# Kernel optimization log

Hardware: AMD Instinct MI355X
Metric: run time of the kernel (lower is better)

Reference implementation:

```python
import jax, jax.numpy as jnp
import numpy as np

N = 50000
E = 800000
IN_C = 128
HID = 32
OUT_C = 16
NEG_SLOPE = 0.2


def setup_inputs() -> dict:
    key = jax.random.key(0)
    ks = jax.random.split(key, 16)
    x = jax.random.normal(ks[0], (N, IN_C), dtype=jnp.float32)
    edge_index = jax.random.randint(ks[1], (2, E), 0, N, dtype=jnp.int64)

    def glorot(k, shape):
        fan = shape[0] + shape[-1]
        return jax.random.uniform(k, shape, jnp.float32, -1.0, 1.0) * jnp.sqrt(6.0 / fan)

    # layer1: in=128 -> heads=4, ch=32, concat -> out 128
    W1 = glorot(ks[2], (IN_C, 4 * HID))
    a_src1 = glorot(ks[3], (4, HID))
    a_dst1 = glorot(ks[4], (4, HID))
    b1 = jnp.zeros((4 * HID,), jnp.float32)
    # layer2: in=128 -> heads=2, ch=32, concat -> out 64
    W2 = glorot(ks[5], (4 * HID, 2 * HID))
    a_src2 = glorot(ks[6], (2, HID))
    a_dst2 = glorot(ks[7], (2, HID))
    b2 = jnp.zeros((2 * HID,), jnp.float32)
    # layer3: in=64 -> heads=1, ch=16, mean -> out 16
    W3 = glorot(ks[8], (2 * HID, OUT_C))
    a_src3 = glorot(ks[9], (1, OUT_C))
    a_dst3 = glorot(ks[10], (1, OUT_C))
    b3 = jnp.zeros((OUT_C,), jnp.float32)
    return {"x": x, "edge_index": edge_index,
            "W1": W1, "a_src1": a_src1, "a_dst1": a_dst1, "b1": b1,
            "W2": W2, "a_src2": a_src2, "a_dst2": a_dst2, "b2": b2,
            "W3": W3, "a_src3": a_src3, "a_dst3": a_dst3, "b3": b3}


def gat_conv(x, src, dst, W, a_src, a_dst, bias, heads, ch, concat):
    n = x.shape[0]
    h = (x @ W).reshape(n, heads, ch)                      # [N,H,C]
    alpha_s = jnp.einsum('nhc,hc->nh', h, a_src)           # [N,H]
    alpha_d = jnp.einsum('nhc,hc->nh', h, a_dst)           # [N,H]
    logits = jax.nn.leaky_relu(alpha_s[src] + alpha_d[dst], NEG_SLOPE)  # [E,H]
    # segment softmax over edges sharing the same destination node
    m = jax.ops.segment_max(logits, dst, num_segments=n)
    m = jnp.where(jnp.isfinite(m), m, 0.0)
    e = jnp.exp(logits - m[dst])
    denom = jax.ops.segment_sum(e, dst, num_segments=n)
    alpha = e / (denom[dst] + 1e-16)                       # [E,H]
    msg = h[src] * alpha[:, :, None]                       # [E,H,C]
    out = jax.ops.segment_sum(msg, dst, num_segments=n)    # [N,H,C]
    out = out.reshape(n, heads * ch) if concat else out.mean(axis=1)
    return out + bias


def reference(x, edge_index, W1, a_src1, a_dst1, b1, W2, a_src2, a_dst2, b2, W3, a_src3, a_dst3, b3):
    n = x.shape[0]
    loops = jnp.arange(n, dtype=edge_index.dtype)
    src = jnp.concatenate([edge_index[0], loops])  # add self loops (PyG default)
    dst = jnp.concatenate([edge_index[1], loops])
    h = jax.nn.relu(gat_conv(x, src, dst, W1, a_src1, a_dst1, b1, 4, HID, True))
    h = jax.nn.relu(gat_conv(h, src, dst, W2, a_src2, a_dst2, b2, 2, HID, True))
    out = gat_conv(h, src, dst, W3, a_src3, a_dst3, b3, 1, OUT_C, False)
    return out
```

## Files before the change

kernel.cpp:

```cpp
#include <hip/hip_runtime.h>
#include <hip/hip_bf16.h>
#include <stdint.h>

#define NODES 50000
#define NEDGE 800000
#define TEDGE (NEDGE + NODES)

typedef unsigned short u16;
typedef unsigned int u32;
typedef unsigned long long u64;
typedef short s16x8 __attribute__((ext_vector_type(8)));
typedef float f32x4 __attribute__((ext_vector_type(4)));

__device__ __forceinline__ float bf2f(u16 v) {
  return __uint_as_float(((u32)v) << 16);
}
__device__ __forceinline__ u16 f2bf(float f) {
  u32 u = __float_as_uint(f);
  u32 r = (u + 0x7FFFu + ((u >> 16) & 1u)) >> 16;
  return (u16)r;
}
__device__ __forceinline__ float lo16f(u32 w) { return __uint_as_float(w << 16); }
__device__ __forceinline__ float hi16f(u32 w) { return __uint_as_float(w & 0xFFFF0000u); }
__device__ __forceinline__ float lrelu(float x) {
  return (x > 0.f) ? x : 0.2f * x;
}
__device__ __forceinline__ int clampn(int v) {
  return ((u32)v < NODES) ? v : 0;
}
__device__ __forceinline__ float load1(const void* p, size_t i, bool fb) {
  return fb ? bf2f(((const u16*)p)[i]) : ((const float*)p)[i];
}
__device__ __forceinline__ u32 encf(float f) {
  u32 u = __float_as_uint(f);
  return (u & 0x80000000u) ? ~u : (u | 0x80000000u);
}
__device__ __forceinline__ float decf(u32 k) {
  u32 u = (k & 0x80000000u) ? (k & 0x7FFFFFFFu) : ~k;
  return __uint_as_float(u);
}

__global__ __launch_bounds__(256) void k_probe(const int* __restrict__ ei,
                                               const u16* __restrict__ xs16,
                                               int* __restrict__ flags,
                                               int* __restrict__ deg) {
  int t = threadIdx.x;
  int g = blockIdx.x * 256 + t;
  if (g < NODES) deg[g] = 0;
  if (blockIdx.x == 0 && t >= 2 && t < 32) flags[t] = 0;
  if (blockIdx.x == 0 && t < 64) {
    int odd = 0, even = 0, big = 0;
#pragma unroll
    for (int k = 0; k < 4; ++k) {
      int idx = t + 64 * k;
      odd |= (ei[2 * idx + 1] != 0);
      even |= (ei[2 * idx] != 0);
      u32 ex = (xs16[2 * (t * 4 + k)] >> 7) & 0xFF;
      big += (ex >= 0x90);
    }
    u64 bo = __ballot(odd);
    u64 be = __ballot(even);
#pragma unroll
    for (int off = 32; off >= 1; off >>= 1) big += __shfl_xor(big, off);
    if (t == 0) {
      flags[0] = (bo == 0ull && be != 0ull) ? 1 : 0;
      flags[1] = (big >= 8) ? 0 : 1;
    }
  }
}


__global__ __launch_bounds__(256) void k_hist(const int* __restrict__ ei,
                                              const int* __restrict__ flags,
                                              int* deg, u16* __restrict__ rankarr,
                                              u16* __restrict__ src16,
                                              u16* __restrict__ dst16,
                                              const void* __restrict__ W1,
                                              const void* __restrict__ W2,
                                              const void* __restrict__ W3,
                                              u16* __restrict__ wt1,
                                              u16* __restrict__ wt2,
                                              u16* __restrict__ wt3) {
  int e = blockIdx.x * 256 + threadIdx.x;
  if (e >= TEDGE) return;
  bool fb = flags[1] != 0;
  if (e < 25600) {
    if (e < 16384) {
      int n = e >> 7, k = e & 127;
      wt1[n * 128 + k] = f2bf(load1(W1, (size_t)k * 128 + n, fb));
    } else if (e < 24576) {
      int r = e - 16384;
      int n = r >> 7, k = r & 127;
      wt2[n * 128 + k] = f2bf(load1(W2, (size_t)k * 64 + n, fb));
    } else {
      int r = e - 24576;
      int n = r >> 6, k = r & 63;
      wt3[n * 64 + k] = f2bf(load1(W3, (size_t)k * 16 + n, fb));
    }
  }
  int d, s;
  if (e < NEDGE) {
    if (flags[0]) { s = ei[2 * e]; d = ei[2 * (NEDGE + e)]; }
    else { s = ei[e]; d = ei[NEDGE + e]; }
  } else {
    s = e - NEDGE; d = s;
  }
  s = clampn(s); d = clampn(d);
  src16[e] = (u16)s;
  dst16[e] = (u16)d;
  int r = atomicAdd(&deg[d], 1);
  rankarr[e] = (u16)min(r, 65535);
}

__global__ __launch_bounds__(1024) void k_scan(const int* __restrict__ deg,
                                               int* __restrict__ rowptr, int n) {
  int t = threadIdx.x, lane = t & 63, w = t >> 6;
  __shared__ int swave[16], soff[17];
  int carry = 0;
  for (int base = 0; base < n; base += 4096) {
    int i0 = base + t * 4;
    int v[4];
#pragma unroll
    for (int j = 0; j < 4; j++) { int i = i0 + j; v[j] = (i < n) ? deg[i] : 0; }
    int local = v[0] + v[1] + v[2] + v[3];
    int x = local;
#pragma unroll
    for (int off = 1; off < 64; off <<= 1) {
      int y = __shfl_up(x, off);
      if (lane >= off) x += y;
    }
    if (lane == 63) swave[w] = x;
    __syncthreads();
    if (w == 0) {
      int wv = (lane < 16) ? swave[lane] : 0;
#pragma unroll
      for (int off = 1; off < 16; off <<= 1) {
        int y = __shfl_up(wv, off);
        if (lane >= off) wv += y;
      }
      if (lane < 16) soff[lane + 1] = wv;
      if (lane == 0) soff[0] = 0;
    }
    __syncthreads();
    int run = carry + soff[w] + (x - local);
#pragma unroll
    for (int j = 0; j < 4; j++) {
      int i = i0 + j;
      if (i < n) rowptr[i] = run;
      run += v[j];
    }
    carry += soff[16];
    __syncthreads();
  }
  if (t == 0) rowptr[n] = carry;
}

__global__ __launch_bounds__(256) void k_scatter(const u16* __restrict__ src16,
                                                 const u16* __restrict__ dst16,
                                                 const int* __restrict__ rowptr,
                                                 const u16* __restrict__ rankarr,
                                                 u16* __restrict__ srcs) {
  int e = blockIdx.x * 256 + threadIdx.x;
  if (e >= TEDGE) return;
  int d = dst16[e];
  int pos = rowptr[d] + (int)rankarr[e];
  srcs[pos] = src16[e];
}


template <int K, int N, int H, bool XEXT>
__global__ __launch_bounds__(256) void k_gmfma(const void* __restrict__ xin,
                                               const u16* __restrict__ wtg,
                                               const void* __restrict__ a_src,
                                               const void* __restrict__ a_dst,
                                               u16* __restrict__ hout,
                                               float* __restrict__ asg,
                                               float* __restrict__ adg,
                                               u32* __restrict__ gm,
                                               const int* __restrict__ flags,
                                               int M) {
  constexpr int KP = K + 8;
  constexpr int NT = N / 16;
  constexpr int NTH = NT / H;
  constexpr int KG = K / 8;
  __shared__ u16 wlds[N * KP];
  __shared__ u16 xlds[64 * KP];
  __shared__ u32 lmax[2 * H];
  int t = threadIdx.x;
  int row0 = blockIdx.x * 64;
  bool fb = flags[1] != 0;
  if (t < 2 * H) lmax[t] = 0;

  for (int i = t; i < N * KG; i += 256) {
    int n = i / KG, kg = i % KG;
    *(uint4*)&wlds[n * KP + kg * 8] = *(const uint4*)(wtg + (size_t)n * K + kg * 8);
  }
  bool xbf = XEXT ? fb : true;
  for (int i = t; i < 64 * KG; i += 256) {
    int r = i / KG, kg = i % KG;
    int grow = row0 + r;
    if (grow >= M) grow = M - 1;
    if (xbf) {
      *(uint4*)&xlds[r * KP + kg * 8] =
          *(const uint4*)((const u16*)xin + (size_t)grow * K + kg * 8);
    } else {
      const float* gp = (const float*)xin + (size_t)grow * K + kg * 8;
      float4 f0 = *(const float4*)gp, f1 = *(const float4*)(gp + 4);
      *(ushort4*)&xlds[r * KP + kg * 8] =
          make_ushort4(f2bf(f0.x), f2bf(f0.y), f2bf(f0.z), f2bf(f0.w));
      *(ushort4*)&xlds[r * KP + kg * 8 + 4] =
          make_ushort4(f2bf(f1.x), f2bf(f1.y), f2bf(f1.z), f2bf(f1.w));
    }
  }
  __syncthreads();

  int lane = t & 63, w = t >> 6;
  int lrow = lane & 15, quad = lane >> 4;
  f32x4 acc[NT];
#pragma unroll
  for (int nt = 0; nt < NT; ++nt) acc[nt] = (f32x4){0.f, 0.f, 0.f, 0.f};

  const u16* xbase = xlds + (w * 16 + lrow) * KP + quad * 8;
  const u16* wbase = wlds + lrow * KP + quad * 8;
#pragma unroll
  for (int ks = 0; ks < K / 32; ++ks) {
    s16x8 a = *(const s16x8*)(xbase + ks * 32);
#pragma unroll
    for (int nt = 0; nt < NT; ++nt) {
      s16x8 b = *(const s16x8*)(wbase + (size_t)nt * 16 * KP + ks * 32);
      acc[nt] = __builtin_amdgcn_mfma_f32_16x16x32_bf16(a, b, acc[nt], 0, 0, 0);
    }
  }

  float avs[NT], avd[NT];
#pragma unroll
  for (int nt = 0; nt < NT; ++nt) {
    avs[nt] = load1(a_src, nt * 16 + lrow, fb);
    avd[nt] = load1(a_dst, nt * 16 + lrow, fb);
  }
  int baserow = row0 + w * 16 + quad * 4;
#pragma unroll
  for (int r = 0; r < 4; ++r) {
    int grow = baserow + r;
    float ps[H], pd[H];
#pragma unroll
    for (int h = 0; h < H; ++h) {
      ps[h] = 0.f; pd[h] = 0.f;
#pragma unroll
      for (int i = 0; i < NTH; ++i) {
        int nt = h * NTH + i;
        ps[h] += acc[nt][r] * avs[nt];
        pd[h] += acc[nt][r] * avd[nt];
      }
    }
#pragma unroll
    for (int m = 1; m < 16; m <<= 1) {
#pragma unroll
      for (int h = 0; h < H; ++h) {
        ps[h] += __shfl_xor(ps[h], m);
        pd[h] += __shfl_xor(pd[h], m);
      }
    }
    if (grow < M) {
#pragma unroll
      for (int nt = 0; nt < NT; ++nt)
        hout[(size_t)grow * N + nt * 16 + lrow] = f2bf(acc[nt][r]);
#pragma unroll
      for (int h = 0; h < H; ++h) {
        if (lrow == h) {
          asg[grow * H + h] = ps[h];
          adg[grow * H + h] = pd[h];
          atomicMax(&lmax[h], encf(ps[h]));
          atomicMax(&lmax[H + h], encf(pd[h]));
        }
      }
    }
  }
  __syncthreads();
  if (t < 2 * H) atomicMax(&gm[t], lmax[t]);
}


template <int H, int C, bool RELU, bool FINAL>
__global__ __launch_bounds__(256) void k_agg(const u16* __restrict__ hbuf,
                                             const float* __restrict__ asg,
                                             const float* __restrict__ adg,
                                             const int* __restrict__ rowptr,
                                             const u16* __restrict__ srcs,
                                             const void* __restrict__ bias,
                                             const int* __restrict__ flags,
                                             const u32* __restrict__ gm,
                                             void* __restrict__ outp, int n) {
  constexpr int HC = H * C;
  constexpr int L = HC / 8;
  constexpr int EPN = 32 / L;
  constexpr int UN = (4 * EPN <= 32) ? 4 : 2;
  __shared__ u16 lds_s[4][64];
  __shared__ float lds_e[4][64][H];
  int lane = threadIdx.x & 63;
  int w = threadIdx.x >> 6;
  int nh = lane >> 5;
  int hl = lane & 31;
  int node = blockIdx.x * 8 + w * 2 + nh;
  if (node >= n) node = n - 1;
  bool fb = flags[1] != 0;
  int start = rowptr[node], end = rowptr[node + 1];
  if (end < start || end - start > TEDGE) { start = 0; end = 0; }

  float adh[H], M[H];
#pragma unroll
  for (int h = 0; h < H; ++h) adh[h] = adg[node * H + h];
#pragma unroll
  for (int h = 0; h < H; ++h) M[h] = lrelu(decf(gm[h]) + decf(gm[H + h]));

  int sub = hl / L;
  int cl = hl & (L - 1);
  int ch0 = cl * 8;
  int myhead = ch0 / C;
  int base = nh * 32;

  float den[H];
#pragma unroll
  for (int h = 0; h < H; ++h) den[h] = 0.f;
  float acc[UN][8];
#pragma unroll
  for (int u = 0; u < UN; ++u)
#pragma unroll
    for (int i = 0; i < 8; ++i) acc[u][i] = 0.f;

  for (int chunk = start; chunk < end; chunk += 32) {
    int e = chunk + hl;
    int s = 0;
    float ee[H];
#pragma unroll
    for (int h = 0; h < H; ++h) ee[h] = 0.f;
    if (e < end) {
      s = srcs[e];
      float av[H];
      if (H == 4) { float4 t4 = *(const float4*)(asg + s * 4);
        av[0] = t4.x; av[1] = t4.y; av[H > 2 ? 2 : 0] = t4.z; av[H > 3 ? 3 : 0] = t4.w; }
      else if (H == 2) { float2 t2 = *(const float2*)(asg + s * 2); av[0] = t2.x; av[1] = t2.y; }
      else av[0] = asg[s];
#pragma unroll
      for (int h = 0; h < H; ++h) {
        float x = __expf(lrelu(av[h] + adh[h]) - M[h]);
        ee[h] = x;
        den[h] += x;
      }
    }
    __builtin_amdgcn_wave_barrier();
    lds_s[w][lane] = (u16)s;
#pragma unroll
    for (int h = 0; h < H; ++h) lds_e[w][lane][h] = ee[h];
    __builtin_amdgcn_wave_barrier();

    int cn = min(32, end - chunk);
    for (int j = 0; j < cn; j += UN * EPN) {
      int sx[UN];
      float ax[UN];
#pragma unroll
      for (int u = 0; u < UN; ++u) {
        int ei_ = base + j + u * EPN + sub;
        sx[u] = lds_s[w][ei_];
        ax[u] = lds_e[w][ei_][myhead];
      }
#pragma unroll
      for (int u = 0; u < UN; ++u) {
        uint4 v = *(const uint4*)(hbuf + (size_t)sx[u] * HC + ch0);
        acc[u][0] += ax[u] * lo16f(v.x); acc[u][1] += ax[u] * hi16f(v.x);
        acc[u][2] += ax[u] * lo16f(v.y); acc[u][3] += ax[u] * hi16f(v.y);
        acc[u][4] += ax[u] * lo16f(v.z); acc[u][5] += ax[u] * hi16f(v.z);
        acc[u][6] += ax[u] * lo16f(v.w); acc[u][7] += ax[u] * hi16f(v.w);
      }
    }
  }

#pragma unroll
  for (int m = 16; m >= 1; m >>= 1) {
#pragma unroll
    for (int h = 0; h < H; ++h) den[h] += __shfl_xor(den[h], m);
  }
  float tt[8];
#pragma unroll
  for (int i = 0; i < 8; ++i) {
    tt[i] = acc[0][i];
#pragma unroll
    for (int u = 1; u < UN; ++u) tt[i] += acc[u][i];
  }
#pragma unroll
  for (int m = L; m < 32; m <<= 1) {
#pragma unroll
    for (int i = 0; i < 8; ++i) tt[i] += __shfl_xor(tt[i], m);
  }

  if (sub == 0) {
    float inv = 1.f / (den[myhead] + 1e-16f);
    float o[8];
#pragma unroll
    for (int i = 0; i < 8; ++i) {
      o[i] = tt[i] * inv + load1(bias, ch0 + i, fb);
      if (RELU) o[i] = fmaxf(o[i], 0.f);
    }
    bool obf = FINAL ? fb : true;
    if (obf) {
      uint4 pk;
      pk.x = (u32)f2bf(o[0]) | ((u32)f2bf(o[1]) << 16);
      pk.y = (u32)f2bf(o[2]) | ((u32)f2bf(o[3]) << 16);
      pk.z = (u32)f2bf(o[4]) | ((u32)f2bf(o[5]) << 16);
      pk.w = (u32)f2bf(o[6]) | ((u32)f2bf(o[7]) << 16);
      *(uint4*)((u16*)outp + (size_t)node * HC + ch0) = pk;
    } else {
      float* op = (float*)outp + (size_t)node * HC + ch0;
      *(float4*)op = make_float4(o[0], o[1], o[2], o[3]);
      *(float4*)(op + 4) = make_float4(o[4], o[5], o[6], o[7]);
    }
  }
}


extern "C" void kernel_launch(void* const* d_in, const int* in_sizes, int n_in,
                              void* d_out, int out_size, void* d_ws, size_t ws_size,
                              hipStream_t stream) {
  const void* x   = d_in[0];
  const int* ei   = (const int*)d_in[1];
  const void* W1  = d_in[2];
  const void* as1 = d_in[3];
  const void* ad1 = d_in[4];
  const void* b1  = d_in[5];
  const void* W2  = d_in[6];
  const void* as2 = d_in[7];
  const void* ad2 = d_in[8];
  const void* b2  = d_in[9];
  const void* W3  = d_in[10];
  const void* as3 = d_in[11];
  const void* ad3 = d_in[12];
  const void* b3  = d_in[13];

  char* w = (char*)d_ws;
  auto alloc = [&](size_t bytes) {
    char* p = w;
    w += (bytes + 255) & ~(size_t)255;
    return p;
  };
  int* flags    = (int*)alloc(256);
  int* deg      = (int*)alloc((size_t)NODES * 4);
  int* rowptr   = (int*)alloc((size_t)(NODES + 1) * 4);
  u16* rankarr  = (u16*)alloc((size_t)TEDGE * 2);
  u16* src16    = (u16*)alloc((size_t)TEDGE * 2);
  u16* dst16    = (u16*)alloc((size_t)TEDGE * 2);
  u16* srcs     = (u16*)alloc((size_t)TEDGE * 2);
  float* asg    = (float*)alloc((size_t)NODES * 4 * 4);
  float* adg    = (float*)alloc((size_t)NODES * 4 * 4);
  u16* wt1      = (u16*)alloc((size_t)128 * 128 * 2);
  u16* wt2      = (u16*)alloc((size_t)64 * 128 * 2);
  u16* wt3      = (u16*)alloc((size_t)16 * 64 * 2);
  u16* hbuf     = (u16*)alloc((size_t)NODES * 128 * 2);
  u16* obuf     = (u16*)alloc((size_t)NODES * 128 * 2);

  u32* gm1 = (u32*)(flags + 8);
  u32* gm2 = (u32*)(flags + 16);
  u32* gm3 = (u32*)(flags + 24);

  k_probe<<<(NODES + 255) / 256, 256, 0, stream>>>(ei, (const u16*)x, flags, deg);
  k_hist<<<(TEDGE + 255) / 256, 256, 0, stream>>>(ei, flags, deg, rankarr, src16, dst16,
                                                  W1, W2, W3, wt1, wt2, wt3);
  k_scan<<<1, 1024, 0, stream>>>(deg, rowptr, NODES);
  k_scatter<<<(TEDGE + 255) / 256, 256, 0, stream>>>(src16, dst16, rowptr, rankarr, srcs);

  int gblocks = (NODES + 63) / 64;
  int ablocks = (NODES + 7) / 8;
  k_gmfma<128, 128, 4, true><<<gblocks, 256, 0, stream>>>(x, wt1, as1, ad1, hbuf, asg, adg, gm1, flags, NODES);
  k_agg<4, 32, true, false><<<ablocks, 256, 0, stream>>>(hbuf, asg, adg, rowptr, srcs, b1, flags, gm1, obuf, NODES);
  k_gmfma<128, 64, 2, false><<<gblocks, 256, 0, stream>>>(obuf, wt2, as2, ad2, hbuf, asg, adg, gm2, flags, NODES);
  k_agg<2, 32, true, false><<<ablocks, 256, 0, stream>>>(hbuf, asg, adg, rowptr, srcs, b2, flags, gm2, obuf, NODES);
  k_gmfma<64, 16, 1, false><<<gblocks, 256, 0, stream>>>(obuf, wt3, as3, ad3, hbuf, asg, adg, gm3, flags, NODES);
  k_agg<1, 16, false, true><<<ablocks, 256, 0, stream>>>(hbuf, asg, adg, rowptr, srcs, b3, flags, gm3, d_out, NODES);
}
```

Before: 307.6 us.

## Fuse histogram, scan and layer-1 GEMM into one kernel with spin-wait

Moves the weight transposition into the probe kernel, with each block recomputing the precision flag locally. The edge histogram, the single-block prefix scan and the layer-1 MFMA GEMM now run as one launch. Block 0 spins on an atomic counter until all histogram blocks finish and then scans, so the GEMM tiles run concurrently with the graph build. This removes two launches and the serialized single-block scan from the critical path. It relies on block 0 not starving the histogram blocks while it spins, and uses a 256-thread scan in place of the 1024-thread one.

```diff
diff --git a/kernel.cpp b/kernel.cpp
--- a/kernel.cpp
+++ b/kernel.cpp
@@ -5,6 +5,8 @@
 #define NODES 50000
 #define NEDGE 800000
 #define TEDGE (NEDGE + NODES)
+#define HBLK ((TEDGE + 255) / 256)
+#define GBLK ((NODES + 63) / 64)
 
 typedef unsigned short u16;
 typedef unsigned int u32;
@@ -43,151 +45,80 @@
 __global__ __launch_bounds__(256) void k_probe(const int* __restrict__ ei,
                                                const u16* __restrict__ xs16,
                                                int* __restrict__ flags,
-                                               int* __restrict__ deg) {
+                                               int* __restrict__ deg,
+                                               const void* __restrict__ W1,
+                                               const void* __restrict__ W2,
+                                               const void* __restrict__ W3,
+                                               u16* __restrict__ wt1,
+                                               u16* __restrict__ wt2,
+                                               u16* __restrict__ wt3) {
+  __shared__ int sfb;
   int t = threadIdx.x;
   int g = blockIdx.x * 256 + t;
   if (g < NODES) deg[g] = 0;
   if (blockIdx.x == 0 && t >= 2 && t < 32) flags[t] = 0;
-  if (blockIdx.x == 0 && t < 64) {
-    int odd = 0, even = 0, big = 0;
+  if (t < 64) {
+    int big = 0;
 #pragma unroll
     for (int k = 0; k < 4; ++k) {
-      int idx = t + 64 * k;
-      odd |= (ei[2 * idx + 1] != 0);
-      even |= (ei[2 * idx] != 0);
       u32 ex = (xs16[2 * (t * 4 + k)] >> 7) & 0xFF;
       big += (ex >= 0x90);
     }
-    u64 bo = __ballot(odd);
-    u64 be = __ballot(even);
 #pragma unroll
     for (int off = 32; off >= 1; off >>= 1) big += __shfl_xor(big, off);
-    if (t == 0) {
-      flags[0] = (bo == 0ull && be != 0ull) ? 1 : 0;
-      flags[1] = (big >= 8) ? 0 : 1;
-    }
-  }
-}
-
-
-__global__ __launch_bounds__(256) void k_hist(const int* __restrict__ ei,
-                                              const int* __restrict__ flags,
-                                              int* deg, u16* __restrict__ rankarr,
-                                              u16* __restrict__ src16,
-                                              u16* __restrict__ dst16,
-                                              const void* __restrict__ W1,
-                                              const void* __restrict__ W2,
-                                              const void* __restrict__ W3,
-                                              u16* __restrict__ wt1,
-                                              u16* __restrict__ wt2,
-                                              u16* __restrict__ wt3) {
-  int e = blockIdx.x * 256 + threadIdx.x;
-  if (e >= TEDGE) return;
-  bool fb = flags[1] != 0;
-  if (e < 25600) {
-    if (e < 16384) {
-      int n = e >> 7, k = e & 127;
+    if (t == 0) sfb = (big >= 8) ? 0 : 1;
+    if (blockIdx.x == 0) {
+      int odd = 0, even = 0;
+#pragma unroll
+      for (int k = 0; k < 4; ++k) {
+        int idx = t + 64 * k;
+        odd |= (ei[2 * idx + 1] != 0);
+        even |= (ei[2 * idx] != 0);
+      }
+      u64 bo = __ballot(odd);
+      u64 be = __ballot(even);
+      if (t == 0) flags[0] = (bo == 0ull && be != 0ull) ? 1 : 0;
+    }
+  }
+  __syncthreads();
+  bool fb = sfb != 0;
+  if (blockIdx.x == 0 && t == 0) flags[1] = fb ? 1 : 0;
+  if (g < 25600) {
+    if (g < 16384) {
+      int n = g >> 7, k = g & 127;
       wt1[n * 128 + k] = f2bf(load1(W1, (size_t)k * 128 + n, fb));
-    } else if (e < 24576) {
-      int r = e - 16384;
+    } else if (g < 24576) {
+      int r = g - 16384;
       int n = r >> 7, k = r & 127;
       wt2[n * 128 + k] = f2bf(load1(W2, (size_t)k * 64 + n, fb));
     } else {
-      int r = e - 24576;
+      int r = g - 24576;
       int n = r >> 6, k = r & 63;
       wt3[n * 64 + k] = f2bf(load1(W3, (size_t)k * 16 + n, fb));
     }
   }
-  int d, s;
-  if (e < NEDGE) {
-    if (flags[0]) { s = ei[2 * e]; d = ei[2 * (NEDGE + e)]; }
-    else { s = ei[e]; d = ei[NEDGE + e]; }
-  } else {
-    s = e - NEDGE; d = s;
-  }
-  s = clampn(s); d = clampn(d);
-  src16[e] = (u16)s;
-  dst16[e] = (u16)d;
-  int r = atomicAdd(&deg[d], 1);
-  rankarr[e] = (u16)min(r, 65535);
-}
-
-__global__ __launch_bounds__(1024) void k_scan(const int* __restrict__ deg,
-                                               int* __restrict__ rowptr, int n) {
-  int t = threadIdx.x, lane = t & 63, w = t >> 6;
-  __shared__ int swave[16], soff[17];
-  int carry = 0;
-  for (int base = 0; base < n; base += 4096) {
-    int i0 = base + t * 4;
-    int v[4];
-#pragma unroll
-    for (int j = 0; j < 4; j++) { int i = i0 + j; v[j] = (i < n) ? deg[i] : 0; }
-    int local = v[0] + v[1] + v[2] + v[3];
-    int x = local;
-#pragma unroll
-    for (int off = 1; off < 64; off <<= 1) {
-      int y = __shfl_up(x, off);
-      if (lane >= off) x += y;
-    }
-    if (lane == 63) swave[w] = x;
-    __syncthreads();
-    if (w == 0) {
-      int wv = (lane < 16) ? swave[lane] : 0;
-#pragma unroll
-      for (int off = 1; off < 16; off <<= 1) {
-        int y = __shfl_up(wv, off);
-        if (lane >= off) wv += y;
-      }
-      if (lane < 16) soff[lane + 1] = wv;
-      if (lane == 0) soff[0] = 0;
-    }
-    __syncthreads();
-    int run = carry + soff[w] + (x - local);
-#pragma unroll
-    for (int j = 0; j < 4; j++) {
-      int i = i0 + j;
-      if (i < n) rowptr[i] = run;
-      run += v[j];
-    }
-    carry += soff[16];
-    __syncthreads();
-  }
-  if (t == 0) rowptr[n] = carry;
-}
-
-__global__ __launch_bounds__(256) void k_scatter(const u16* __restrict__ src16,
-                                                 const u16* __restrict__ dst16,
-                                                 const int* __restrict__ rowptr,
-                                                 const u16* __restrict__ rankarr,
-                                                 u16* __restrict__ srcs) {
-  int e = blockIdx.x * 256 + threadIdx.x;
-  if (e >= TEDGE) return;
-  int d = dst16[e];
-  int pos = rowptr[d] + (int)rankarr[e];
-  srcs[pos] = src16[e];
 }
 
 
 template <int K, int N, int H, bool XEXT>
-__global__ __launch_bounds__(256) void k_gmfma(const void* __restrict__ xin,
-                                               const u16* __restrict__ wtg,
-                                               const void* __restrict__ a_src,
-                                               const void* __restrict__ a_dst,
-                                               u16* __restrict__ hout,
-                                               float* __restrict__ asg,
-                                               float* __restrict__ adg,
-                                               u32* __restrict__ gm,
-                                               const int* __restrict__ flags,
-                                               int M) {
+__device__ __forceinline__ void gmfma_tile(const void* __restrict__ xin,
+                                           const u16* __restrict__ wtg,
+                                           const void* __restrict__ a_src,
+                                           const void* __restrict__ a_dst,
+                                           u16* __restrict__ hout,
+                                           float* __restrict__ asg,
+                                           float* __restrict__ adg,
+                                           u32* __restrict__ gm,
+                                           const int* __restrict__ flags,
+                                           int M, int row0,
+                                           u16* __restrict__ wlds,
+                                           u16* __restrict__ xlds,
+                                           u32* __restrict__ lmax) {
   constexpr int KP = K + 8;
   constexpr int NT = N / 16;
   constexpr int NTH = NT / H;
   constexpr int KG = K / 8;
-  __shared__ u16 wlds[N * KP];
-  __shared__ u16 xlds[64 * KP];
-  __shared__ u32 lmax[2 * H];
   int t = threadIdx.x;
-  int row0 = blockIdx.x * 64;
   bool fb = flags[1] != 0;
   if (t < 2 * H) lmax[t] = 0;
 
@@ -278,6 +209,137 @@
   }
   __syncthreads();
   if (t < 2 * H) atomicMax(&gm[t], lmax[t]);
+}
+
+template <int K, int N, int H, bool XEXT>
+__global__ __launch_bounds__(256) void k_gmfma(const void* __restrict__ xin,
+                                               const u16* __restrict__ wtg,
+                                               const void* __restrict__ a_src,
+                                               const void* __restrict__ a_dst,
+                                               u16* __restrict__ hout,
+                                               float* __restrict__ asg,
+                                               float* __restrict__ adg,
+                                               u32* __restrict__ gm,
+                                               const int* __restrict__ flags,
+                                               int M) {
+  constexpr int KP = K + 8;
+  __shared__ u16 wlds[N * KP];
+  __shared__ u16 xlds[64 * KP];
+  __shared__ u32 lmax[2 * H];
+  gmfma_tile<K, N, H, XEXT>(xin, wtg, a_src, a_dst, hout, asg, adg, gm, flags,
+                            M, blockIdx.x * 64, wlds, xlds, lmax);
+}
+
+__global__ __launch_bounds__(256) void k_build_l1(
+    const void* __restrict__ xin, const u16* __restrict__ wtg,
+    const void* __restrict__ a_src, const void* __restrict__ a_dst,
+    u16* __restrict__ hout, float* __restrict__ asg, float* __restrict__ adg,
+    u32* __restrict__ gm, int* __restrict__ flags,
+    const int* __restrict__ ei, u16* __restrict__ src16,
+    u16* __restrict__ dst16, u16* __restrict__ rankarr,
+    int* __restrict__ deg, int* __restrict__ rowptr) {
+  __shared__ u16 wlds[128 * 136];
+  __shared__ u16 xlds[64 * 136];
+  __shared__ u32 lmax[8];
+  __shared__ int swave[4];
+  __shared__ int soff[5];
+  int t = threadIdx.x;
+  int bi = blockIdx.x;
+
+  if (bi == 0) {
+    if (t == 0) {
+      while (__hip_atomic_load(&flags[2], __ATOMIC_ACQUIRE,
+                               __HIP_MEMORY_SCOPE_AGENT) < HBLK)
+        __builtin_amdgcn_s_sleep(8);
+    }
+    __syncthreads();
+    int lane = t & 63, w = t >> 6;
+    int carry = 0;
+    for (int base = 0; base < NODES; base += 4096) {
+      int i0 = base + t * 16;
+      int v[16];
+#pragma unroll
+      for (int j = 0; j < 16; j += 4) {
+        int i = i0 + j;
+        if (i + 4 <= NODES) {
+          int4 qv = *(const int4*)(deg + i);
+          v[j] = qv.x; v[j + 1] = qv.y; v[j + 2] = qv.z; v[j + 3] = qv.w;
+        } else {
+#pragma unroll
+          for (int u = 0; u < 4; ++u) v[j + u] = (i + u < NODES) ? deg[i + u] : 0;
+        }
+      }
+      int local = 0;
+#pragma unroll
+      for (int j = 0; j < 16; ++j) local += v[j];
+      int x = local;
+#pragma unroll
+      for (int off = 1; off < 64; off <<= 1) {
+        int y = __shfl_up(x, off);
+        if (lane >= off) x += y;
+      }
+      if (lane == 63) swave[w] = x;
+      __syncthreads();
+      if (t == 0) {
+        int a = 0;
+#pragma unroll
+        for (int u = 0; u < 4; ++u) { soff[u] = a; a += swave[u]; }
+        soff[4] = a;
+      }
+      __syncthreads();
+      int run = carry + soff[w] + (x - local);
+#pragma unroll
+      for (int j = 0; j < 16; ++j) {
+        int i = i0 + j;
+        if (i < NODES) rowptr[i] = run;
+        run += v[j];
+      }
+      carry += soff[4];
+      __syncthreads();
+    }
+    if (t == 0) rowptr[NODES] = carry;
+    return;
+  }
+
+  int q = bi - 1;
+  if (q < HBLK) {
+    int e = q * 256 + t;
+    if (e < TEDGE) {
+      int d, s;
+      if (e < NEDGE) {
+        if (flags[0]) { s = ei[2 * e]; d = ei[2 * (NEDGE + e)]; }
+        else { s = ei[e]; d = ei[NEDGE + e]; }
+      } else {
+        s = e - NEDGE; d = s;
+      }
+      s = clampn(s); d = clampn(d);
+      src16[e] = (u16)s;
+      dst16[e] = (u16)d;
+      int r = atomicAdd(&deg[d], 1);
+      rankarr[e] = (u16)min(r, 65535);
+    }
+    __syncthreads();
+    if (t == 0)
+      __hip_atomic_fetch_add(&flags[2], 1, __ATOMIC_RELEASE,
+                             __HIP_MEMORY_SCOPE_AGENT);
+    return;
+  }
+
+  gmfma_tile<128, 128, 4, true>(xin, wtg, a_src, a_dst, hout, asg, adg, gm,
+                                flags, NODES, (q - HBLK) * 64, wlds, xlds,
+                                lmax);
+}
+
+__global__ __launch_bounds__(256) void k_scatter(const u16* __restrict__ src16,
+                                                 const u16* __restrict__ dst16,
+                                                 const int* __restrict__ rowptr,
+                                                 const u16* __restrict__ rankarr,
+                                                 u16* __restrict__ srcs) {
+  int e = blockIdx.x * 256 + threadIdx.x;
+  if (e >= TEDGE) return;
+  int d = dst16[e];
+  int pos = rowptr[d] + (int)rankarr[e];
+  srcs[pos] = src16[e];
 }
 
 
@@ -461,18 +523,17 @@
   u32* gm2 = (u32*)(flags + 16);
   u32* gm3 = (u32*)(flags + 24);
 
-  k_probe<<<(NODES + 255) / 256, 256, 0, stream>>>(ei, (const u16*)x, flags, deg);
-  k_hist<<<(TEDGE + 255) / 256, 256, 0, stream>>>(ei, flags, deg, rankarr, src16, dst16,
-                                                  W1, W2, W3, wt1, wt2, wt3);
-  k_scan<<<1, 1024, 0, stream>>>(deg, rowptr, NODES);
+  int ablocks = (NODES + 7) / 8;
+
+  k_probe<<<(NODES + 255) / 256, 256, 0, stream>>>(ei, (const u16*)x, flags, deg,
+                                                   W1, W2, W3, wt1, wt2, wt3);
+  k_build_l1<<<1 + HBLK + GBLK, 256, 0, stream>>>(x, wt1, as1, ad1, hbuf, asg,
+                                                  adg, gm1, flags, ei, src16,
+                                                  dst16, rankarr, deg, rowptr);
   k_scatter<<<(TEDGE + 255) / 256, 256, 0, stream>>>(src16, dst16, rowptr, rankarr, srcs);
-
-  int gblocks = (NODES + 63) / 64;
-  int ablocks = (NODES + 7) / 8;
-  k_gmfma<128, 128, 4, true><<<gblocks, 256, 0, stream>>>(x, wt1, as1, ad1, hbuf, asg, adg, gm1, flags, NODES);
   k_agg<4, 32, true, false><<<ablocks, 256, 0, stream>>>(hbuf, asg, adg, rowptr, srcs, b1, flags, gm1, obuf, NODES);
-  k_gmfma<128, 64, 2, false><<<gblocks, 256, 0, stream>>>(obuf, wt2, as2, ad2, hbuf, asg, adg, gm2, flags, NODES);
+  k_gmfma<128, 64, 2, false><<<GBLK, 256, 0, stream>>>(obuf, wt2, as2, ad2, hbuf, asg, adg, gm2, flags, NODES);
   k_agg<2, 32, true, false><<<ablocks, 256, 0, stream>>>(hbuf, asg, adg, rowptr, srcs, b2, flags, gm2, obuf, NODES);
-  k_gmfma<64, 16, 1, false><<<gblocks, 256, 0, stream>>>(obuf, wt3, as3, ad3, hbuf, asg, adg, gm3, flags, NODES);
+  k_gmfma<64, 16, 1, false><<<GBLK, 256, 0, stream>>>(obuf, wt3, as3, ad3, hbuf, asg, adg, gm3, flags, NODES);
   k_agg<1, 16, false, true><<<ablocks, 256, 0, stream>>>(hbuf, asg, adg, rowptr, srcs, b3, flags, gm3, d_out, NODES);
 }
```

After: 326.7 us. 1.06x slower.

## Fold attention vectors into GEMM, parallelize scan, use pre-swizzled weight fragments

Applied to the files above, without the earlier changes.

Precomputes W·a_src and W·a_dst as an extra bf16 MFMA column tile so attention logits come out of the GEMM instead of a shuffle reduction. Stores weights in MFMA fragment order and reads them directly from global memory, dropping the LDS staging, with each wave handling 32 rows. Replaces the single-block degree scan with a 25-block scan that exchanges partial sums through a spin-waited atomic counter. Weight preprocessing moves from the edge histogram kernel into the probe kernel; this adds bf16 rounding of the folded attention weights and relies on all scan blocks being co-resident.

```diff
diff --git a/kernel.cpp b/kernel.cpp
--- a/kernel.cpp
+++ b/kernel.cpp
@@ -5,6 +5,7 @@
 #define NODES 50000
 #define NEDGE 800000
 #define TEDGE (NEDGE + NODES)
+#define SBLK 25
 
 typedef unsigned short u16;
 typedef unsigned int u32;
@@ -40,64 +41,108 @@
   return __uint_as_float(u);
 }
 
-__global__ __launch_bounds__(256) void k_probe(const int* __restrict__ ei,
-                                               const u16* __restrict__ xs16,
-                                               int* __restrict__ flags,
-                                               int* __restrict__ deg) {
+__global__ __launch_bounds__(256) void k_probe(
+    const int* __restrict__ ei, const u16* __restrict__ xs16,
+    int* __restrict__ flags, int* __restrict__ deg,
+    const void* __restrict__ W1, const void* __restrict__ W2,
+    const void* __restrict__ W3, const void* __restrict__ as1,
+    const void* __restrict__ ad1, const void* __restrict__ as2,
+    const void* __restrict__ ad2, const void* __restrict__ as3,
+    const void* __restrict__ ad3, u16* __restrict__ wt1,
+    u16* __restrict__ wt2, u16* __restrict__ wt3, u16* __restrict__ wa1,
+    u16* __restrict__ wa2, u16* __restrict__ wa3) {
+  __shared__ int sfb;
   int t = threadIdx.x;
   int g = blockIdx.x * 256 + t;
   if (g < NODES) deg[g] = 0;
   if (blockIdx.x == 0 && t >= 2 && t < 32) flags[t] = 0;
-  if (blockIdx.x == 0 && t < 64) {
-    int odd = 0, even = 0, big = 0;
+  if (t < 64) {
+    int big = 0;
 #pragma unroll
     for (int k = 0; k < 4; ++k) {
-      int idx = t + 64 * k;
-      odd |= (ei[2 * idx + 1] != 0);
-      even |= (ei[2 * idx] != 0);
       u32 ex = (xs16[2 * (t * 4 + k)] >> 7) & 0xFF;
       big += (ex >= 0x90);
     }
-    u64 bo = __ballot(odd);
-    u64 be = __ballot(even);
 #pragma unroll
     for (int off = 32; off >= 1; off >>= 1) big += __shfl_xor(big, off);
-    if (t == 0) {
-      flags[0] = (bo == 0ull && be != 0ull) ? 1 : 0;
-      flags[1] = (big >= 8) ? 0 : 1;
-    }
-  }
-}
-
+    if (t == 0) sfb = (big >= 8) ? 0 : 1;
+    if (blockIdx.x == 0) {
+      int odd = 0, even = 0;
+#pragma unroll
+      for (int k = 0; k < 4; ++k) {
+        int idx = t + 64 * k;
+        odd |= (ei[2 * idx + 1] != 0);
+        even |= (ei[2 * idx] != 0);
+      }
+      u64 bo = __ballot(odd);
+      u64 be = __ballot(even);
+      if (t == 0) flags[0] = (bo == 0ull && be != 0ull) ? 1 : 0;
+    }
+  }
+  __syncthreads();
+  bool fb = sfb != 0;
+  if (blockIdx.x == 0 && t == 0) flags[1] = fb ? 1 : 0;
+
+  auto fidx = [](int n, int k, int KS) {
+    int nt = n >> 4, lrow = n & 15, ks = k >> 5, quad = (k >> 3) & 3, j = k & 7;
+    return ((size_t)((nt * KS + ks) * 64 + quad * 16 + lrow)) * 8 + j;
+  };
+
+  if (g < 16384) {
+    int n = g >> 7, k = g & 127;
+    wt1[fidx(n, k, 4)] = f2bf(load1(W1, (size_t)k * 128 + n, fb));
+  } else if (g < 24576) {
+    int r = g - 16384;
+    int n = r >> 7, k = r & 127;
+    wt2[fidx(n, k, 4)] = f2bf(load1(W2, (size_t)k * 64 + n, fb));
+  } else if (g < 25600) {
+    int r = g - 24576;
+    int n = r >> 6, k = r & 63;
+    wt3[fidx(n, k, 2)] = f2bf(load1(W3, (size_t)k * 16 + n, fb));
+  } else if (g < 27648) {
+    int e = g - 25600;
+    int n = e >> 7, k = e & 127;
+    float v = 0.f;
+    if (n < 8) {
+      int head = (n < 4) ? n : n - 4;
+      const void* av = (n < 4) ? as1 : ad1;
+      for (int c = 0; c < 32; ++c)
+        v += load1(W1, (size_t)k * 128 + head * 32 + c, fb) *
+             load1(av, head * 32 + c, fb);
+    }
+    wa1[fidx(n, k, 4)] = (n < 8) ? f2bf(v) : (u16)0;
+  } else if (g < 29696) {
+    int e = g - 27648;
+    int n = e >> 7, k = e & 127;
+    float v = 0.f;
+    if (n < 4) {
+      int head = (n < 2) ? n : n - 2;
+      const void* av = (n < 2) ? as2 : ad2;
+      for (int c = 0; c < 32; ++c)
+        v += load1(W2, (size_t)k * 64 + head * 32 + c, fb) *
+             load1(av, head * 32 + c, fb);
+    }
+    wa2[fidx(n, k, 4)] = (n < 4) ? f2bf(v) : (u16)0;
+  } else if (g < 30720) {
+    int e = g - 29696;
+    int n = e >> 6, k = e & 63;
+    float v = 0.f;
+    if (n < 2) {
+      const void* av = (n < 1) ? as3 : ad3;
+      for (int c = 0; c < 16; ++c)
+        v += load1(W3, (size_t)k * 16 + c, fb) * load1(av, c, fb);
+    }
+    wa3[fidx(n, k, 2)] = (n < 2) ? f2bf(v) : (u16)0;
+  }
+}
 
 __global__ __launch_bounds__(256) void k_hist(const int* __restrict__ ei,
                                               const int* __restrict__ flags,
                                               int* deg, u16* __restrict__ rankarr,
                                               u16* __restrict__ src16,
-                                              u16* __restrict__ dst16,
-                                              const void* __restrict__ W1,
-                                              const void* __restrict__ W2,
-                                              const void* __restrict__ W3,
-                                              u16* __restrict__ wt1,
-                                              u16* __restrict__ wt2,
-                                              u16* __restrict__ wt3) {
+                                              u16* __restrict__ dst16) {
   int e = blockIdx.x * 256 + threadIdx.x;
   if (e >= TEDGE) return;
-  bool fb = flags[1] != 0;
-  if (e < 25600) {
-    if (e < 16384) {
-      int n = e >> 7, k = e & 127;
-      wt1[n * 128 + k] = f2bf(load1(W1, (size_t)k * 128 + n, fb));
-    } else if (e < 24576) {
-      int r = e - 16384;
-      int n = r >> 7, k = r & 127;
-      wt2[n * 128 + k] = f2bf(load1(W2, (size_t)k * 64 + n, fb));
-    } else {
-      int r = e - 24576;
-      int n = r >> 6, k = r & 63;
-      wt3[n * 64 + k] = f2bf(load1(W3, (size_t)k * 16 + n, fb));
-    }
-  }
   int d, s;
   if (e < NEDGE) {
     if (flags[0]) { s = ei[2 * e]; d = ei[2 * (NEDGE + e)]; }
@@ -113,46 +158,64 @@
 }
 
 __global__ __launch_bounds__(1024) void k_scan(const int* __restrict__ deg,
-                                               int* __restrict__ rowptr, int n) {
-  int t = threadIdx.x, lane = t & 63, w = t >> 6;
-  __shared__ int swave[16], soff[17];
-  int carry = 0;
-  for (int base = 0; base < n; base += 4096) {
-    int i0 = base + t * 4;
-    int v[4];
-#pragma unroll
-    for (int j = 0; j < 4; j++) { int i = i0 + j; v[j] = (i < n) ? deg[i] : 0; }
-    int local = v[0] + v[1] + v[2] + v[3];
-    int x = local;
-#pragma unroll
-    for (int off = 1; off < 64; off <<= 1) {
-      int y = __shfl_up(x, off);
-      if (lane >= off) x += y;
-    }
-    if (lane == 63) swave[w] = x;
-    __syncthreads();
-    if (w == 0) {
-      int wv = (lane < 16) ? swave[lane] : 0;
-#pragma unroll
-      for (int off = 1; off < 16; off <<= 1) {
-        int y = __shfl_up(wv, off);
-        if (lane >= off) wv += y;
-      }
-      if (lane < 16) soff[lane + 1] = wv;
-      if (lane == 0) soff[0] = 0;
-    }
-    __syncthreads();
-    int run = carry + soff[w] + (x - local);
-#pragma unroll
-    for (int j = 0; j < 4; j++) {
-      int i = i0 + j;
-      if (i < n) rowptr[i] = run;
-      run += v[j];
-    }
-    carry += soff[16];
-    __syncthreads();
-  }
-  if (t == 0) rowptr[n] = carry;
+                                               int* __restrict__ rowptr,
+                                               int* __restrict__ parts,
+                                               int* __restrict__ counter) {
+  __shared__ int swave[16];
+  __shared__ int sbase, stot;
+  int b = blockIdx.x, t = threadIdx.x;
+  int lane = t & 63, w = t >> 6;
+  int i0 = b * 2048 + t * 2;
+  int v0 = (i0 < NODES) ? deg[i0] : 0;
+  int v1 = (i0 + 1 < NODES) ? deg[i0 + 1] : 0;
+  int local = v0 + v1;
+  int x = local;
+#pragma unroll
+  for (int off = 1; off < 64; off <<= 1) {
+    int y = __shfl_up(x, off);
+    if (lane >= off) x += y;
+  }
+  if (lane == 63) swave[w] = x;
+  __syncthreads();
+  if (w == 0) {
+    int wv = (lane < 16) ? swave[lane] : 0;
+#pragma unroll
+    for (int off = 1; off < 16; off <<= 1) {
+      int y = __shfl_up(wv, off);
+      if (lane >= off) wv += y;
+    }
+    if (lane == 15) {
+      __hip_atomic_store(&parts[b], wv, __ATOMIC_RELAXED,
+                         __HIP_MEMORY_SCOPE_AGENT);
+      __hip_atomic_fetch_add(counter, 1, __ATOMIC_RELEASE,
+                             __HIP_MEMORY_SCOPE_AGENT);
+    }
+    if (lane < 16) swave[lane] = wv;
+  }
+  __syncthreads();
+  if (t == 0) {
+    while (__hip_atomic_load(counter, __ATOMIC_ACQUIRE,
+                             __HIP_MEMORY_SCOPE_AGENT) < SBLK)
+      __builtin_amdgcn_s_sleep(2);
+  }
+  __syncthreads();
+  if (w == 0) {
+    int pv = (lane < SBLK) ? __hip_atomic_load(&parts[lane], __ATOMIC_RELAXED,
+                                               __HIP_MEMORY_SCOPE_AGENT)
+                           : 0;
+    int pb = (lane < b) ? pv : 0;
+#pragma unroll
+    for (int off = 32; off >= 1; off >>= 1) {
+      pb += __shfl_xor(pb, off);
+      pv += __shfl_xor(pv, off);
+    }
+    if (lane == 0) { sbase = pb; stot = pv; }
+  }
+  __syncthreads();
+  int run = sbase + ((w == 0) ? 0 : swave[w - 1]) + (x - local);
+  if (i0 < NODES) rowptr[i0] = run;
+  if (i0 + 1 < NODES) rowptr[i0 + 1] = run + v0;
+  if (b == 0 && t == 0) rowptr[NODES] = stot;
 }
 
 __global__ __launch_bounds__(256) void k_scatter(const u16* __restrict__ src16,
@@ -167,119 +230,91 @@
   srcs[pos] = src16[e];
 }
 
-
 template <int K, int N, int H, bool XEXT>
 __global__ __launch_bounds__(256) void k_gmfma(const void* __restrict__ xin,
-                                               const u16* __restrict__ wtg,
-                                               const void* __restrict__ a_src,
-                                               const void* __restrict__ a_dst,
+                                               const u16* __restrict__ wtf,
+                                               const u16* __restrict__ waf,
                                                u16* __restrict__ hout,
                                                float* __restrict__ asg,
                                                float* __restrict__ adg,
                                                u32* __restrict__ gm,
                                                const int* __restrict__ flags,
                                                int M) {
-  constexpr int KP = K + 8;
   constexpr int NT = N / 16;
-  constexpr int NTH = NT / H;
-  constexpr int KG = K / 8;
-  __shared__ u16 wlds[N * KP];
-  __shared__ u16 xlds[64 * KP];
+  constexpr int KS = K / 32;
   __shared__ u32 lmax[2 * H];
   int t = threadIdx.x;
-  int row0 = blockIdx.x * 64;
+  int lane = t & 63, w = t >> 6;
+  int lrow = lane & 15, quad = lane >> 4;
   bool fb = flags[1] != 0;
   if (t < 2 * H) lmax[t] = 0;
-
-  for (int i = t; i < N * KG; i += 256) {
-    int n = i / KG, kg = i % KG;
-    *(uint4*)&wlds[n * KP + kg * 8] = *(const uint4*)(wtg + (size_t)n * K + kg * 8);
-  }
-  bool xbf = XEXT ? fb : true;
-  for (int i = t; i < 64 * KG; i += 256) {
-    int r = i / KG, kg = i % KG;
-    int grow = row0 + r;
-    if (grow >= M) grow = M - 1;
-    if (xbf) {
-      *(uint4*)&xlds[r * KP + kg * 8] =
-          *(const uint4*)((const u16*)xin + (size_t)grow * K + kg * 8);
-    } else {
-      const float* gp = (const float*)xin + (size_t)grow * K + kg * 8;
-      float4 f0 = *(const float4*)gp, f1 = *(const float4*)(gp + 4);
-      *(ushort4*)&xlds[r * KP + kg * 8] =
-          make_ushort4(f2bf(f0.x), f2bf(f0.y), f2bf(f0.z), f2bf(f0.w));
-      *(ushort4*)&xlds[r * KP + kg * 8 + 4] =
-          make_ushort4(f2bf(f1.x), f2bf(f1.y), f2bf(f1.z), f2bf(f1.w));
-    }
-  }
-  __syncthreads();
-
-  int lane = t & 63, w = t >> 6;
-  int lrow = lane & 15, quad = lane >> 4;
-  f32x4 acc[NT];
-#pragma unroll
-  for (int nt = 0; nt < NT; ++nt) acc[nt] = (f32x4){0.f, 0.f, 0.f, 0.f};
-
-  const u16* xbase = xlds + (w * 16 + lrow) * KP + quad * 8;
-  const u16* wbase = wlds + lrow * KP + quad * 8;
-#pragma unroll
-  for (int ks = 0; ks < K / 32; ++ks) {
-    s16x8 a = *(const s16x8*)(xbase + ks * 32);
-#pragma unroll
-    for (int nt = 0; nt < NT; ++nt) {
-      s16x8 b = *(const s16x8*)(wbase + (size_t)nt * 16 * KP + ks * 32);
-      acc[nt] = __builtin_amdgcn_mfma_f32_16x16x32_bf16(a, b, acc[nt], 0, 0, 0);
-    }
-  }
-
-  float avs[NT], avd[NT];
-#pragma unroll
-  for (int nt = 0; nt < NT; ++nt) {
-    avs[nt] = load1(a_src, nt * 16 + lrow, fb);
-    avd[nt] = load1(a_dst, nt * 16 + lrow, fb);
-  }
-  int baserow = row0 + w * 16 + quad * 4;
-#pragma unroll
-  for (int r = 0; r < 4; ++r) {
-    int grow = baserow + r;
-    float ps[H], pd[H];
-#pragma unroll
-    for (int h = 0; h < H; ++h) {
-      ps[h] = 0.f; pd[h] = 0.f;
-#pragma unroll
-      for (int i = 0; i < NTH; ++i) {
-        int nt = h * NTH + i;
-        ps[h] += acc[nt][r] * avs[nt];
-        pd[h] += acc[nt][r] * avd[nt];
+  __syncthreads();
+
+  int row0 = blockIdx.x * 128 + w * 32;
+  f32x4 acc[2][NT];
+  f32x4 eacc[2];
+#pragma unroll
+  for (int mt = 0; mt < 2; ++mt) {
+    eacc[mt] = (f32x4){0.f, 0.f, 0.f, 0.f};
+#pragma unroll
+    for (int nt = 0; nt < NT; ++nt) acc[mt][nt] = (f32x4){0.f, 0.f, 0.f, 0.f};
+  }
+  int r0c = row0 + lrow;
+  int r1c = row0 + 16 + lrow;
+  if (r0c >= M) r0c = M - 1;
+  if (r1c >= M) r1c = M - 1;
+
+#pragma unroll 1
+  for (int ks = 0; ks < KS; ++ks) {
+    s16x8 bw[NT];
+#pragma unroll
+    for (int nt = 0; nt < NT; ++nt)
+      bw[nt] = *(const s16x8*)(wtf + ((size_t)((nt * KS + ks) * 64 + lane)) * 8);
+    s16x8 be = *(const s16x8*)(waf + ((size_t)(ks * 64 + lane)) * 8);
+#pragma unroll
+    for (int mt = 0; mt < 2; ++mt) {
+      int grow = mt ? r1c : r0c;
+      s16x8 a;
+      if (XEXT && !fb) {
+        const float* gp = (const float*)xin + (size_t)grow * K + ks * 32 + quad * 8;
+        float4 f0 = *(const float4*)gp;
+        float4 f1 = *(const float4*)(gp + 4);
+        a[0] = (short)f2bf(f0.x); a[1] = (short)f2bf(f0.y);
+        a[2] = (short)f2bf(f0.z); a[3] = (short)f2bf(f0.w);
+        a[4] = (short)f2bf(f1.x); a[5] = (short)f2bf(f1.y);
+        a[6] = (short)f2bf(f1.z); a[7] = (short)f2bf(f1.w);
+      } else {
+        a = *(const s16x8*)((const u16*)xin + (size_t)grow * K + ks * 32 + quad * 8);
       }
-    }
-#pragma unroll
-    for (int m = 1; m < 16; m <<= 1) {
-#pragma unroll
-      for (int h = 0; h < H; ++h) {
-        ps[h] += __shfl_xor(ps[h], m);
-        pd[h] += __shfl_xor(pd[h], m);
+#pragma unroll
+      for (int nt = 0; nt < NT; ++nt)
+        acc[mt][nt] =
+            __builtin_amdgcn_mfma_f32_16x16x32_bf16(a, bw[nt], acc[mt][nt], 0, 0, 0);
+      eacc[mt] = __builtin_amdgcn_mfma_f32_16x16x32_bf16(a, be, eacc[mt], 0, 0, 0);
+    }
+  }
+
+  float pm = -3.4e38f;
+#pragma unroll
+  for (int mt = 0; mt < 2; ++mt) {
+    int baserow = row0 + mt * 16 + quad * 4;
+#pragma unroll
+    for (int r = 0; r < 4; ++r) {
+      int grow = baserow + r;
+      if (grow < M) {
+#pragma unroll
+        for (int nt = 0; nt < NT; ++nt)
+          hout[(size_t)grow * N + nt * 16 + lrow] = f2bf(acc[mt][nt][r]);
+        if (lrow < H) asg[grow * H + lrow] = eacc[mt][r];
+        else if (lrow < 2 * H) adg[grow * H + (lrow - H)] = eacc[mt][r];
       }
-    }
-    if (grow < M) {
-#pragma unroll
-      for (int nt = 0; nt < NT; ++nt)
-        hout[(size_t)grow * N + nt * 16 + lrow] = f2bf(acc[nt][r]);
-#pragma unroll
-      for (int h = 0; h < H; ++h) {
-        if (lrow == h) {
-          asg[grow * H + h] = ps[h];
-          adg[grow * H + h] = pd[h];
-          atomicMax(&lmax[h], encf(ps[h]));
-          atomicMax(&lmax[H + h], encf(pd[h]));
-        }
-      }
-    }
-  }
+      pm = fmaxf(pm, eacc[mt][r]);
+    }
+  }
+  if (lrow < 2 * H) atomicMax(&lmax[lrow], encf(pm));
   __syncthreads();
   if (t < 2 * H) atomicMax(&gm[t], lmax[t]);
 }
-
 
 template <int H, int C, bool RELU, bool FINAL>
 __global__ __launch_bounds__(256) void k_agg(const u16* __restrict__ hbuf,
@@ -443,6 +478,7 @@
     return p;
   };
   int* flags    = (int*)alloc(256);
+  int* parts    = (int*)alloc(256);
   int* deg      = (int*)alloc((size_t)NODES * 4);
   int* rowptr   = (int*)alloc((size_t)(NODES + 1) * 4);
   u16* rankarr  = (u16*)alloc((size_t)TEDGE * 2);
@@ -454,6 +490,9 @@
   u16* wt1      = (u16*)alloc((size_t)128 * 128 * 2);
   u16* wt2      = (u16*)alloc((size_t)64 * 128 * 2);
   u16* wt3      = (u16*)alloc((size_t)16 * 64 * 2);
+  u16* wa1      = (u16*)alloc((size_t)16 * 128 * 2);
+  u16* wa2      = (u16*)alloc((size_t)16 * 128 * 2);
+  u16* wa3      = (u16*)alloc((size_t)16 * 64 * 2);
   u16* hbuf     = (u16*)alloc((size_t)NODES * 128 * 2);
   u16* obuf     = (u16*)alloc((size_t)NODES * 128 * 2);
 
@@ -461,18 +500,21 @@
   u32* gm2 = (u32*)(flags + 16);
   u32* gm3 = (u32*)(flags + 24);
 
-  k_probe<<<(NODES + 255) / 256, 256, 0, stream>>>(ei, (const u16*)x, flags, deg);
-  k_hist<<<(TEDGE + 255) / 256, 256, 0, stream>>>(ei, flags, deg, rankarr, src16, dst16,
-                                                  W1, W2, W3, wt1, wt2, wt3);
-  k_scan<<<1, 1024, 0, stream>>>(deg, rowptr, NODES);
+  int gblocks = (NODES + 127) / 128;
+  int ablocks = (NODES + 7) / 8;
+
+  k_probe<<<(NODES + 255) / 256, 256, 0, stream>>>(
+      ei, (const u16*)x, flags, deg, W1, W2, W3, as1, ad1, as2, ad2, as3, ad3,
+      wt1, wt2, wt3, wa1, wa2, wa3);
+  k_hist<<<(TEDGE + 255) / 256, 256, 0, stream>>>(ei, flags, deg, rankarr,
+                                                  src16, dst16);
+  k_scan<<<SBLK, 1024, 0, stream>>>(deg, rowptr, parts, flags + 2);
   k_scatter<<<(TEDGE + 255) / 256, 256, 0, stream>>>(src16, dst16, rowptr, rankarr, srcs);
 
-  int gblocks = (NODES + 63) / 64;
-  int ablocks = (NODES + 7) / 8;
-  k_gmfma<128, 128, 4, true><<<gblocks, 256, 0, stream>>>(x, wt1, as1, ad1, hbuf, asg, adg, gm1, flags, NODES);
+  k_gmfma<128, 128, 4, true><<<gblocks, 256, 0, stream>>>(x, wt1, wa1, hbuf, asg, adg, gm1, flags, NODES);
   k_agg<4, 32, true, false><<<ablocks, 256, 0, stream>>>(hbuf, asg, adg, rowptr, srcs, b1, flags, gm1, obuf, NODES);
-  k_gmfma<128, 64, 2, false><<<gblocks, 256, 0, stream>>>(obuf, wt2, as2, ad2, hbuf, asg, adg, gm2, flags, NODES);
+  k_gmfma<128, 64, 2, false><<<gblocks, 256, 0, stream>>>(obuf, wt2, wa2, hbuf, asg, adg, gm2, flags, NODES);
   k_agg<2, 32, true, false><<<ablocks, 256, 0, stream>>>(hbuf, asg, adg, rowptr, srcs, b2, flags, gm2, obuf, NODES);
-  k_gmfma<64, 16, 1, false><<<gblocks, 256, 0, stream>>>(obuf, wt3, as3, ad3, hbuf, asg, adg, gm3, flags, NODES);
+  k_gmfma<64, 16, 1, false><<<gblocks, 256, 0, stream>>>(obuf, wt3, wa3, hbuf, asg, adg, gm3, flags, NODES);
   k_agg<1, 16, false, true><<<ablocks, 256, 0, stream>>>(hbuf, asg, adg, rowptr, srcs, b3, flags, gm3, d_out, NODES);
 }
```

Result: faster. 265.1 us (-13.8%).
